# Performance work log

Hardware: AMD Instinct MI355X
Metric: run time of the kernel (lower is better)

Reference implementation:

```python
import jax, jax.numpy as jnp
import numpy as np

N = 50000
E = 800000
IN_C, HID_C, OUT_C = 128, 96, 96
EPS = 1e-5


def setup_inputs() -> dict:
    key = jax.random.key(0)
    ks = jax.random.split(key, 16)
    s = lambda k, shape, fan: jax.random.normal(k, shape, jnp.float32) / np.sqrt(fan)
    inp = {
        "x": jax.random.normal(ks[0], (N, IN_C), jnp.float32),
        "edge_index": jax.random.randint(ks[1], (2, E), 0, N, jnp.int64),
        # GCNConv weights (x @ W then aggregate, bias added after)
        "W1": s(ks[2], (IN_C, HID_C), IN_C), "b1": jnp.zeros((HID_C,), jnp.float32),
        "W2": s(ks[3], (HID_C, HID_C), HID_C), "b2": jnp.zeros((HID_C,), jnp.float32),
        "W3": s(ks[4], (HID_C, OUT_C), HID_C), "b3": jnp.zeros((OUT_C,), jnp.float32),
        # BatchNorm affine params
        "g1": jnp.ones((HID_C,), jnp.float32), "bt1": jnp.zeros((HID_C,), jnp.float32),
        "g2": jnp.ones((HID_C,), jnp.float32), "bt2": jnp.zeros((HID_C,), jnp.float32),
        "g3": jnp.ones((OUT_C,), jnp.float32), "bt3": jnp.zeros((OUT_C,), jnp.float32),
        # MLP head
        "fw1": s(ks[5], (OUT_C, 128), OUT_C), "fb1": jnp.zeros((128,), jnp.float32),
        "fw2": s(ks[6], (128, 64), 128), "fb2": jnp.zeros((64,), jnp.float32),
        "fw3": s(ks[7], (64, 32), 64), "fb3": jnp.zeros((32,), jnp.float32),
        "fw4": s(ks[8], (32, 1), 32), "fb4": jnp.zeros((1,), jnp.float32),
    }
    return inp


def gcn_conv(x, W, b, src, dst, n):
    # PyG GCNConv: h = x @ W; add self-loops; sym-normalized scatter-add; + bias
    h = x @ W  # [N, C]
    deg = jax.ops.segment_sum(jnp.ones(src.shape[0], h.dtype), dst, num_segments=n) + 1.0
    dinv = jax.lax.rsqrt(deg)  # deg >= 1 via self-loop
    norm = dinv[src] * dinv[dst]  # [E]
    agg = jax.ops.segment_sum(h[src] * norm[:, None], dst, num_segments=n)
    return agg + h * (dinv * dinv)[:, None] + b  # self-loop term + bias


def batch_norm(x, g, b):
    m = x.mean(axis=0)
    v = x.var(axis=0)  # biased, as torch BN uses in normalization
    return (x - m) * jax.lax.rsqrt(v + EPS) * g + b


def reference(x, edge_index, W1, b1, W2, b2, W3, b3, g1, bt1, g2, bt2, g3, bt3,
              fw1, fb1, fw2, fb2, fw3, fb3, fw4, fb4):
    src, dst = edge_index[0], edge_index[1]
    n = x.shape[0]
    h = jax.nn.relu(batch_norm(gcn_conv(x, W1, b1, src, dst, n), g1, bt1))
    h = jax.nn.relu(batch_norm(gcn_conv(h, W2, b2, src, dst, n), g2, bt2))
    h = jax.nn.relu(batch_norm(gcn_conv(h, W3, b3, src, dst, n), g3, bt3))
    v = h.mean(axis=0)  # graph mean-pool -> [OUT_C]
    v = jax.nn.relu(v @ fw1 + fb1)  # dropout is identity in eval mode
    v = jax.nn.relu(v @ fw2 + fb2)
    v = jax.nn.relu(v @ fw3 + fb3)
    return v @ fw4 + fb4  # [1]
```

## Files before the change

kernel.cpp:

```cpp
#include <hip/hip_runtime.h>
#include <math.h>

#define NCH 96
#define SCAN_TILE 2048

__global__ void zero_kernel(int* __restrict__ cnt, float* __restrict__ small,
                            int n, int nsmall) {
    int i = blockIdx.x * blockDim.x + threadIdx.x;
    if (i < n) cnt[i] = 0;
    if (i < nsmall) small[i] = 0.0f;
}

__global__ void count_kernel(const int* __restrict__ dst, int* __restrict__ cnt, int E) {
    int e = blockIdx.x * blockDim.x + threadIdx.x;
    if (e < E) atomicAdd(&cnt[dst[e]], 1);
}

__global__ __launch_bounds__(256) void scanA_kernel(const int* __restrict__ cnt,
                                                    int* __restrict__ bsum, int n) {
    int b = blockIdx.x, t = threadIdx.x;
    int base = b * SCAN_TILE;
    int s = 0;
    for (int i = t; i < SCAN_TILE; i += 256) {
        int idx = base + i;
        if (idx < n) s += cnt[idx];
    }
#pragma unroll
    for (int off = 32; off; off >>= 1) s += __shfl_down(s, off, 64);
    __shared__ int red[4];
    if ((t & 63) == 0) red[t >> 6] = s;
    __syncthreads();
    if (t == 0) bsum[b] = red[0] + red[1] + red[2] + red[3];
}

__global__ __launch_bounds__(256) void scanB_kernel(int* __restrict__ bsum,
                                                    int* __restrict__ rowptrN, int nb) {
    int t = threadIdx.x;
    __shared__ int ps[256];
    int v = (t < nb) ? bsum[t] : 0;
    ps[t] = v;
    __syncthreads();
    for (int off = 1; off < 256; off <<= 1) {
        int add = (t >= off) ? ps[t - off] : 0;
        __syncthreads();
        ps[t] += add;
        __syncthreads();
    }
    if (t < nb) bsum[t] = ps[t] - v;
    if (t == nb - 1) rowptrN[0] = ps[t];
}

__global__ __launch_bounds__(256) void scanC_kernel(int* __restrict__ cnt,
                                                    const int* __restrict__ bsum,
                                                    int* __restrict__ rowptr,
                                                    float* __restrict__ dinv, int n) {
    int b = blockIdx.x, t = threadIdx.x;
    int base = b * SCAN_TILE + t * 8;
    int c[8];
    int s = 0;
#pragma unroll
    for (int j = 0; j < 8; ++j) {
        int idx = base + j;
        c[j] = (idx < n) ? cnt[idx] : 0;
        s += c[j];
    }
    __shared__ int ps[256];
    ps[t] = s;
    __syncthreads();
    for (int off = 1; off < 256; off <<= 1) {
        int add = (t >= off) ? ps[t - off] : 0;
        __syncthreads();
        ps[t] += add;
        __syncthreads();
    }
    int run = bsum[b] + ps[t] - s;
#pragma unroll
    for (int j = 0; j < 8; ++j) {
        int idx = base + j;
        if (idx < n) {
            rowptr[idx] = run;
            cnt[idx] = run;
            dinv[idx] = rsqrtf((float)(c[j] + 1));
            run += c[j];
        }
    }
}

__global__ void fill_kernel(const int* __restrict__ ei, int* __restrict__ fill,
                            int* __restrict__ adj, int E) {
    int e = blockIdx.x * blockDim.x + threadIdx.x;
    if (e < E) {
        int s = ei[e];
        int pos = atomicAdd(&fill[ei[E + e]], 1);
        adj[pos] = s;
    }
}

template <int K, bool BN>
__global__ __launch_bounds__(256) void gemm_hs(const float* __restrict__ x,
                                               const float* __restrict__ ab,
                                               const float* __restrict__ W,
                                               const float* __restrict__ dinv,
                                               float* __restrict__ hs, int n) {
    __shared__ float Wl[K * NCH];
    __shared__ float Xl[32 * 32];
    __shared__ float ABl[2 * NCH];
    const int tid = threadIdx.y * 32 + threadIdx.x;
    for (int i = tid; i < K * NCH; i += 256) Wl[i] = W[i];
    if (BN && tid < 2 * NCH) ABl[tid] = ab[tid];

    const int r0 = blockIdx.x * 32;
    const int c0 = threadIdx.x;
    const int ry = threadIdx.y;
    float a[4][3] = {};

    for (int kc = 0; kc < K; kc += 32) {
        __syncthreads();
        for (int i = tid; i < 32 * 32; i += 256) {
            int row = i >> 5, kk = i & 31;
            int r = r0 + row;
            float v = (r < n) ? x[(size_t)r * K + kc + kk] : 0.0f;
            if (BN) v = fmaxf(fmaf(v, ABl[kc + kk], ABl[NCH + kc + kk]), 0.0f);
            Xl[i] = v;
        }
        __syncthreads();
#pragma unroll
        for (int kk = 0; kk < 32; ++kk) {
            float w0 = Wl[(kc + kk) * NCH + c0];
            float w1 = Wl[(kc + kk) * NCH + c0 + 32];
            float w2 = Wl[(kc + kk) * NCH + c0 + 64];
#pragma unroll
            for (int j = 0; j < 4; ++j) {
                float xv = Xl[(ry + 8 * j) * 32 + kk];
                a[j][0] = fmaf(xv, w0, a[j][0]);
                a[j][1] = fmaf(xv, w1, a[j][1]);
                a[j][2] = fmaf(xv, w2, a[j][2]);
            }
        }
    }

#pragma unroll
    for (int j = 0; j < 4; ++j) {
        int r = r0 + ry + 8 * j;
        if (r < n) {
            float dv = dinv[r];
#pragma unroll
            for (int i2 = 0; i2 < 3; ++i2)
                hs[(size_t)r * NCH + c0 + 32 * i2] = a[j][i2] * dv;
        }
    }
}

__global__ __launch_bounds__(256) void gather_kernel(const int* __restrict__ rowptr,
                                                     const int* __restrict__ adj,
                                                     const float* __restrict__ dinv,
                                                     const float4* __restrict__ HS,
                                                     float4* __restrict__ AGG, int n) {
    int wid = (blockIdx.x * 256 + threadIdx.x) >> 6;
    int lane = threadIdx.x & 63;
    if (wid >= n || lane >= 24) return;
    int lo = rowptr[wid], hi = rowptr[wid + 1];
    float dv = dinv[wid];
    size_t l = lane;

    float4 a = HS[(size_t)wid * 24 + l];
    float4 b = make_float4(0.f, 0.f, 0.f, 0.f);
    int j = lo;
    for (; j + 1 < hi; j += 2) {
        int s0 = adj[j], s1 = adj[j + 1];
        float4 v0 = HS[(size_t)s0 * 24 + l];
        float4 v1 = HS[(size_t)s1 * 24 + l];
        a.x += v0.x; a.y += v0.y; a.z += v0.z; a.w += v0.w;
        b.x += v1.x; b.y += v1.y; b.z += v1.z; b.w += v1.w;
    }
    if (j < hi) {
        int s0 = adj[j];
        float4 v0 = HS[(size_t)s0 * 24 + l];
        a.x += v0.x; a.y += v0.y; a.z += v0.z; a.w += v0.w;
    }
    a.x = (a.x + b.x) * dv;
    a.y = (a.y + b.y) * dv;
    a.z = (a.z + b.z) * dv;
    a.w = (a.w + b.w) * dv;
    AGG[(size_t)wid * 24 + l] = a;
}

__global__ __launch_bounds__(384) void stats_kernel(const float* __restrict__ t,
                                                    float* __restrict__ sums, int n) {
    int c = threadIdx.x;
    int ry = threadIdx.y;
    float s1 = 0.f, s2 = 0.f;
    for (int r = blockIdx.x * 4 + ry; r < n; r += gridDim.x * 4) {
        float v = t[(size_t)r * NCH + c];
        s1 += v;
        s2 = fmaf(v, v, s2);
    }
    __shared__ float L1[4][NCH], L2[4][NCH];
    L1[ry][c] = s1;
    L2[ry][c] = s2;
    __syncthreads();
    if (ry == 0) {
        s1 = L1[0][c] + L1[1][c] + L1[2][c] + L1[3][c];
        s2 = L2[0][c] + L2[1][c] + L2[2][c] + L2[3][c];
        atomicAdd(&sums[c], s1);
        atomicAdd(&sums[NCH + c], s2);
    }
}

__global__ void bnparam_kernel(const float* __restrict__ sums,
                               const float* __restrict__ g,
                               const float* __restrict__ bt,
                               float* __restrict__ ab, float n) {
    int c = threadIdx.x;
    if (c < NCH) {
        float mean = sums[c] / n;
        float var = sums[NCH + c] / n - mean * mean;
        float a = g[c] * rsqrtf(var + 1e-5f);
        ab[c] = a;
        ab[NCH + c] = bt[c] - mean * a;
    }
}

__global__ __launch_bounds__(384) void apply_pool_kernel(const float* __restrict__ t,
                                                         const float* __restrict__ ab,
                                                         float* __restrict__ pool, int n) {
    int c = threadIdx.x, ry = threadIdx.y;
    float a = ab[c], b = ab[NCH + c];
    float s = 0.f;
    for (int r = blockIdx.x * 4 + ry; r < n; r += gridDim.x * 4) {
        float v = t[(size_t)r * NCH + c];
        s += fmaxf(fmaf(v, a, b), 0.f);
    }
    __shared__ float L[4][NCH];
    L[ry][c] = s;
    __syncthreads();
    if (ry == 0) atomicAdd(&pool[c], L[0][c] + L[1][c] + L[2][c] + L[3][c]);
}

__global__ __launch_bounds__(128) void mlp_kernel(const float* __restrict__ pool,
        const float* __restrict__ fw1, const float* __restrict__ fb1,
        const float* __restrict__ fw2, const float* __restrict__ fb2,
        const float* __restrict__ fw3, const float* __restrict__ fb3,
        const float* __restrict__ fw4, const float* __restrict__ fb4,
        float* __restrict__ out, float invn) {
    __shared__ float v[NCH], l1[128], l2[64], l3[32];
    int t = threadIdx.x;
    if (t < NCH) v[t] = pool[t] * invn;
    __syncthreads();
    {
        float a = fb1[t];
        for (int k = 0; k < NCH; ++k) a = fmaf(v[k], fw1[k * 128 + t], a);
        l1[t] = fmaxf(a, 0.f);
    }
    __syncthreads();
    if (t < 64) {
        float a = fb2[t];
        for (int k = 0; k < 128; ++k) a = fmaf(l1[k], fw2[k * 64 + t], a);
        l2[t] = fmaxf(a, 0.f);
    }
    __syncthreads();
    if (t < 32) {
        float a = fb3[t];
        for (int k = 0; k < 64; ++k) a = fmaf(l2[k], fw3[k * 32 + t], a);
        l3[t] = fmaxf(a, 0.f);
    }
    __syncthreads();
    if (t == 0) {
        float a = fb4[0];
        for (int k = 0; k < 32; ++k) a = fmaf(l3[k], fw4[k], a);
        out[0] = a;
    }
}

extern "C" void kernel_launch(void* const* d_in, const int* in_sizes, int n_in,
                              void* d_out, int out_size, void* d_ws, size_t ws_size,
                              hipStream_t stream) {
    const float* x  = (const float*)d_in[0];
    const int*  ei  = (const int*)d_in[1];
    const float* W1 = (const float*)d_in[2];
    const float* W2 = (const float*)d_in[4];
    const float* W3 = (const float*)d_in[6];
    const float* g1 = (const float*)d_in[8],  *bt1 = (const float*)d_in[9];
    const float* g2 = (const float*)d_in[10], *bt2 = (const float*)d_in[11];
    const float* g3 = (const float*)d_in[12], *bt3 = (const float*)d_in[13];
    const float* fw1 = (const float*)d_in[14], *fb1 = (const float*)d_in[15];
    const float* fw2 = (const float*)d_in[16], *fb2 = (const float*)d_in[17];
    const float* fw3 = (const float*)d_in[18], *fb3 = (const float*)d_in[19];
    const float* fw4 = (const float*)d_in[20], *fb4 = (const float*)d_in[21];
    float* out = (float*)d_out;

    const int N = in_sizes[0] / 128;
    const int E = in_sizes[1] / 2;
    const size_t n96 = (size_t)N * NCH;

    float* ws    = (float*)d_ws;
    float* B0    = ws;
    float* B1    = B0 + n96;
    float* dinv  = B1 + n96;
    float* sums1 = dinv + N;
    float* sums2 = sums1 + 2 * NCH;
    float* sums3 = sums2 + 2 * NCH;
    float* pool  = sums3 + 2 * NCH;
    float* ab1   = pool + NCH;
    float* ab2   = ab1 + 2 * NCH;
    float* ab3   = ab2 + 2 * NCH;
    int*   cnt   = (int*)(ab3 + 2 * NCH);
    int*   rowptr= cnt + N;
    int*   adj   = rowptr + N + 1;
    int*   bsum  = adj + E;
    const int nsmall = 3 * 2 * NCH + NCH;

    dim3 b96(NCH, 4);
    const int gemmGrid = (N + 31) / 32;
    const int gathGrid = (N + 3) / 4;
    const int nb = (N + SCAN_TILE - 1) / SCAN_TILE;

    zero_kernel<<<(N + 255) / 256, 256, 0, stream>>>(cnt, sums1, N, nsmall);
    count_kernel<<<(E + 255) / 256, 256, 0, stream>>>(ei + E, cnt, E);
    scanA_kernel<<<nb, 256, 0, stream>>>(cnt, bsum, N);
    scanB_kernel<<<1, 256, 0, stream>>>(bsum, rowptr + N, nb);
    scanC_kernel<<<nb, 256, 0, stream>>>(cnt, bsum, rowptr, dinv, N);
    fill_kernel<<<(E + 255) / 256, 256, 0, stream>>>(ei, cnt, adj, E);

    gemm_hs<128, false><<<gemmGrid, dim3(32, 8), 0, stream>>>(x, nullptr, W1, dinv, B0, N);
    gather_kernel<<<gathGrid, 256, 0, stream>>>(rowptr, adj, dinv,
                                                (const float4*)B0, (float4*)B1, N);
    stats_kernel<<<512, b96, 0, stream>>>(B1, sums1, N);
    bnparam_kernel<<<1, NCH, 0, stream>>>(sums1, g1, bt1, ab1, (float)N);

    gemm_hs<96, true><<<gemmGrid, dim3(32, 8), 0, stream>>>(B1, ab1, W2, dinv, B0, N);
    gather_kernel<<<gathGrid, 256, 0, stream>>>(rowptr, adj, dinv,
                                                (const float4*)B0, (float4*)B1, N);
    stats_kernel<<<512, b96, 0, stream>>>(B1, sums2, N);
    bnparam_kernel<<<1, NCH, 0, stream>>>(sums2, g2, bt2, ab2, (float)N);

    gemm_hs<96, true><<<gemmGrid, dim3(32, 8), 0, stream>>>(B1, ab2, W3, dinv, B0, N);
    gather_kernel<<<gathGrid, 256, 0, stream>>>(rowptr, adj, dinv,
                                                (const float4*)B0, (float4*)B1, N);
    stats_kernel<<<512, b96, 0, stream>>>(B1, sums3, N);
    bnparam_kernel<<<1, NCH, 0, stream>>>(sums3, g3, bt3, ab3, (float)N);

    apply_pool_kernel<<<512, b96, 0, stream>>>(B1, ab3, pool, N);
    mlp_kernel<<<1, 128, 0, stream>>>(pool, fw1, fb1, fw2, fb2, fw3, fb3,
                                      fw4, fb4, out, 1.0f / (float)N);
}
```

Measured before the change: 558.9 us.

## Use split-bf16 MFMA for GEMMs and store gathered features as bf16

Replaces the scalar FMA GEMM with an MFMA 16x16x32 bf16 kernel. It uses a three-term hi/lo bf16 split to keep near-fp32 accuracy, with weights pre-swizzled into LDS fragment order and 128 rows per block. The GEMM output h*dinv is now stored as bf16, which halves the bytes the random-access neighbor gather reads. The gather accumulates in fp32 after unpacking. The risk is the precision loss from rounding the gathered features to bf16, plus extra conversion work in the GEMM.

After: 500.1 us. 10.5% less time.

```diff
diff --git a/kernel.cpp b/kernel.cpp
--- a/kernel.cpp
+++ b/kernel.cpp
@@ -3,6 +3,25 @@
 
 #define NCH 96
 #define SCAN_TILE 2048
+
+typedef __attribute__((ext_vector_type(8))) short short8;
+typedef __attribute__((ext_vector_type(4))) float f32x4;
+typedef unsigned short ushort_t;
+typedef unsigned int uint_t;
+
+__device__ __forceinline__ uint_t bf16_rne(float f) {
+    uint_t u = __builtin_bit_cast(uint_t, f);
+    return (u + 0x7FFFu + ((u >> 16) & 1u)) >> 16;
+}
+
+__device__ __forceinline__ float4 unp(uint2 u) {
+    float4 r;
+    r.x = __builtin_bit_cast(float, u.x << 16);
+    r.y = __builtin_bit_cast(float, u.x & 0xFFFF0000u);
+    r.z = __builtin_bit_cast(float, u.y << 16);
+    r.w = __builtin_bit_cast(float, u.y & 0xFFFF0000u);
+    return r;
+}
 
 __global__ void zero_kernel(int* __restrict__ cnt, float* __restrict__ small,
                             int n, int nsmall) {
@@ -97,56 +116,99 @@
 }
 
 template <int K, bool BN>
-__global__ __launch_bounds__(256) void gemm_hs(const float* __restrict__ x,
-                                               const float* __restrict__ ab,
-                                               const float* __restrict__ W,
-                                               const float* __restrict__ dinv,
-                                               float* __restrict__ hs, int n) {
-    __shared__ float Wl[K * NCH];
-    __shared__ float Xl[32 * 32];
+__global__ __launch_bounds__(256) void gemm_mfma(const float* __restrict__ x,
+                                                 const float* __restrict__ ab,
+                                                 const float* __restrict__ W,
+                                                 const float* __restrict__ dinv,
+                                                 ushort_t* __restrict__ hs, int n) {
+    constexpr int NKS = K / 32;
+    constexpr int NFR = NKS * 6 * 512;
+    __shared__ short BH[NFR];
+    __shared__ short BL[NFR];
     __shared__ float ABl[2 * NCH];
-    const int tid = threadIdx.y * 32 + threadIdx.x;
-    for (int i = tid; i < K * NCH; i += 256) Wl[i] = W[i];
-    if (BN && tid < 2 * NCH) ABl[tid] = ab[tid];
-
-    const int r0 = blockIdx.x * 32;
-    const int c0 = threadIdx.x;
-    const int ry = threadIdx.y;
-    float a[4][3] = {};
-
-    for (int kc = 0; kc < K; kc += 32) {
-        __syncthreads();
-        for (int i = tid; i < 32 * 32; i += 256) {
-            int row = i >> 5, kk = i & 31;
-            int r = r0 + row;
-            float v = (r < n) ? x[(size_t)r * K + kc + kk] : 0.0f;
-            if (BN) v = fmaxf(fmaf(v, ABl[kc + kk], ABl[NCH + kc + kk]), 0.0f);
-            Xl[i] = v;
+
+    const int tid = threadIdx.x;
+    for (int idx = tid; idx < NFR; idx += 256) {
+        int i  = idx & 7;
+        int l2 = (idx >> 3) & 63;
+        int r  = idx >> 9;
+        int ct = r % 6;
+        int ks = r / 6;
+        int k   = ks * 32 + ((l2 >> 4) << 3) + i;
+        int col = ct * 16 + (l2 & 15);
+        float w = W[k * NCH + col];
+        uint_t hb = bf16_rne(w);
+        float hf = __builtin_bit_cast(float, hb << 16);
+        uint_t lb = bf16_rne(w - hf);
+        BH[idx] = (short)hb;
+        BL[idx] = (short)lb;
+    }
+    if constexpr (BN) {
+        if (tid < 2 * NCH) ABl[tid] = ab[tid];
+    }
+    __syncthreads();
+
+    const int l  = tid & 63;
+    const int wv = tid >> 6;
+    const int r0 = blockIdx.x * 128 + wv * 32;
+    const int klo = (l >> 4) << 3;
+
+    f32x4 acc[2][6] = {};
+
+    for (int ks = 0; ks < NKS; ++ks) {
+        float av[8], bv[8];
+        if constexpr (BN) {
+            int kb = ks * 32 + klo;
+#pragma unroll
+            for (int i = 0; i < 8; ++i) { av[i] = ABl[kb + i]; bv[i] = ABl[NCH + kb + i]; }
         }
-        __syncthreads();
-#pragma unroll
-        for (int kk = 0; kk < 32; ++kk) {
-            float w0 = Wl[(kc + kk) * NCH + c0];
-            float w1 = Wl[(kc + kk) * NCH + c0 + 32];
-            float w2 = Wl[(kc + kk) * NCH + c0 + 64];
-#pragma unroll
-            for (int j = 0; j < 4; ++j) {
-                float xv = Xl[(ry + 8 * j) * 32 + kk];
-                a[j][0] = fmaf(xv, w0, a[j][0]);
-                a[j][1] = fmaf(xv, w1, a[j][1]);
-                a[j][2] = fmaf(xv, w2, a[j][2]);
+        short8 Ah[2], Al[2];
+#pragma unroll
+        for (int rt = 0; rt < 2; ++rt) {
+            int rg = r0 + rt * 16 + (l & 15);
+            rg = rg < n ? rg : n - 1;
+            const float* px = x + (size_t)rg * K + ks * 32 + klo;
+            float4 f0 = *(const float4*)px;
+            float4 f1 = *(const float4*)(px + 4);
+            float vv[8] = {f0.x, f0.y, f0.z, f0.w, f1.x, f1.y, f1.z, f1.w};
+#pragma unroll
+            for (int i = 0; i < 8; ++i) {
+                float v = vv[i];
+                if constexpr (BN) v = fmaxf(fmaf(v, av[i], bv[i]), 0.0f);
+                uint_t hb = bf16_rne(v);
+                float hf = __builtin_bit_cast(float, hb << 16);
+                uint_t lb = bf16_rne(v - hf);
+                Ah[rt][i] = (short)hb;
+                Al[rt][i] = (short)lb;
             }
         }
-    }
-
-#pragma unroll
-    for (int j = 0; j < 4; ++j) {
-        int r = r0 + ry + 8 * j;
-        if (r < n) {
-            float dv = dinv[r];
-#pragma unroll
-            for (int i2 = 0; i2 < 3; ++i2)
-                hs[(size_t)r * NCH + c0 + 32 * i2] = a[j][i2] * dv;
+#pragma unroll
+        for (int ct = 0; ct < 6; ++ct) {
+            int off = ((ks * 6 + ct) << 9) + (l << 3);
+            short8 bh = *(const short8*)&BH[off];
+            short8 bl = *(const short8*)&BL[off];
+#pragma unroll
+            for (int rt = 0; rt < 2; ++rt) {
+                acc[rt][ct] = __builtin_amdgcn_mfma_f32_16x16x32_bf16(Ah[rt], bh, acc[rt][ct], 0, 0, 0);
+                acc[rt][ct] = __builtin_amdgcn_mfma_f32_16x16x32_bf16(Al[rt], bh, acc[rt][ct], 0, 0, 0);
+                acc[rt][ct] = __builtin_amdgcn_mfma_f32_16x16x32_bf16(Ah[rt], bl, acc[rt][ct], 0, 0, 0);
+            }
+        }
+    }
+
+#pragma unroll
+    for (int rt = 0; rt < 2; ++rt) {
+#pragma unroll
+        for (int i = 0; i < 4; ++i) {
+            int row = r0 + rt * 16 + ((l >> 4) << 2) + i;
+            if (row < n) {
+                float dv = dinv[row];
+#pragma unroll
+                for (int ct = 0; ct < 6; ++ct) {
+                    float v = acc[rt][ct][i] * dv;
+                    hs[(size_t)row * NCH + ct * 16 + (l & 15)] = (ushort_t)bf16_rne(v);
+                }
+            }
         }
     }
 }
@@ -154,35 +216,36 @@
 __global__ __launch_bounds__(256) void gather_kernel(const int* __restrict__ rowptr,
                                                      const int* __restrict__ adj,
                                                      const float* __restrict__ dinv,
-                                                     const float4* __restrict__ HS,
-                                                     float4* __restrict__ AGG, int n) {
+                                                     const ushort_t* __restrict__ HS,
+                                                     float* __restrict__ AGG, int n) {
     int wid = (blockIdx.x * 256 + threadIdx.x) >> 6;
     int lane = threadIdx.x & 63;
     if (wid >= n || lane >= 24) return;
     int lo = rowptr[wid], hi = rowptr[wid + 1];
     float dv = dinv[wid];
-    size_t l = lane;
-
-    float4 a = HS[(size_t)wid * 24 + l];
+    const uint_t* HSu = (const uint_t*)HS;
+    const int l2 = lane * 2;
+
+    float4 a = unp(*(const uint2*)(HSu + (size_t)wid * 48 + l2));
     float4 b = make_float4(0.f, 0.f, 0.f, 0.f);
     int j = lo;
     for (; j + 1 < hi; j += 2) {
         int s0 = adj[j], s1 = adj[j + 1];
-        float4 v0 = HS[(size_t)s0 * 24 + l];
-        float4 v1 = HS[(size_t)s1 * 24 + l];
+        float4 v0 = unp(*(const uint2*)(HSu + (size_t)s0 * 48 + l2));
+        float4 v1 = unp(*(const uint2*)(HSu + (size_t)s1 * 48 + l2));
         a.x += v0.x; a.y += v0.y; a.z += v0.z; a.w += v0.w;
         b.x += v1.x; b.y += v1.y; b.z += v1.z; b.w += v1.w;
     }
     if (j < hi) {
         int s0 = adj[j];
-        float4 v0 = HS[(size_t)s0 * 24 + l];
+        float4 v0 = unp(*(const uint2*)(HSu + (size_t)s0 * 48 + l2));
         a.x += v0.x; a.y += v0.y; a.z += v0.z; a.w += v0.w;
     }
     a.x = (a.x + b.x) * dv;
     a.y = (a.y + b.y) * dv;
     a.z = (a.z + b.z) * dv;
     a.w = (a.w + b.w) * dv;
-    AGG[(size_t)wid * 24 + l] = a;
+    ((float4*)(AGG + (size_t)wid * NCH))[lane] = a;
 }
 
 __global__ __launch_bounds__(384) void stats_kernel(const float* __restrict__ t,
@@ -294,9 +357,9 @@
     const size_t n96 = (size_t)N * NCH;
 
     float* ws    = (float*)d_ws;
-    float* B0    = ws;
-    float* B1    = B0 + n96;
-    float* dinv  = B1 + n96;
+    float* T     = ws;
+    ushort_t* HSB = (ushort_t*)(T + n96);
+    float* dinv  = T + n96 + n96 / 2;
     float* sums1 = dinv + N;
     float* sums2 = sums1 + 2 * NCH;
     float* sums3 = sums2 + 2 * NCH;
@@ -311,7 +374,7 @@
     const int nsmall = 3 * 2 * NCH + NCH;
 
     dim3 b96(NCH, 4);
-    const int gemmGrid = (N + 31) / 32;
+    const int gemmGrid = (N + 127) / 128;
     const int gathGrid = (N + 3) / 4;
     const int nb = (N + SCAN_TILE - 1) / SCAN_TILE;
 
@@ -322,25 +385,22 @@
     scanC_kernel<<<nb, 256, 0, stream>>>(cnt, bsum, rowptr, dinv, N);
     fill_kernel<<<(E + 255) / 256, 256, 0, stream>>>(ei, cnt, adj, E);
 
-    gemm_hs<128, false><<<gemmGrid, dim3(32, 8), 0, stream>>>(x, nullptr, W1, dinv, B0, N);
-    gather_kernel<<<gathGrid, 256, 0, stream>>>(rowptr, adj, dinv,
-                                                (const float4*)B0, (float4*)B1, N);
-    stats_kernel<<<512, b96, 0, stream>>>(B1, sums1, N);
+    gemm_mfma<128, false><<<gemmGrid, 256, 0, stream>>>(x, nullptr, W1, dinv, HSB, N);
+    gather_kernel<<<gathGrid, 256, 0, stream>>>(rowptr, adj, dinv, HSB, T, N);
+    stats_kernel<<<512, b96, 0, stream>>>(T, sums1, N);
     bnparam_kernel<<<1, NCH, 0, stream>>>(sums1, g1, bt1, ab1, (float)N);
 
-    gemm_hs<96, true><<<gemmGrid, dim3(32, 8), 0, stream>>>(B1, ab1, W2, dinv, B0, N);
-    gather_kernel<<<gathGrid, 256, 0, stream>>>(rowptr, adj, dinv,
-                                                (const float4*)B0, (float4*)B1, N);
-    stats_kernel<<<512, b96, 0, stream>>>(B1, sums2, N);
+    gemm_mfma<96, true><<<gemmGrid, 256, 0, stream>>>(T, ab1, W2, dinv, HSB, N);
+    gather_kernel<<<gathGrid, 256, 0, stream>>>(rowptr, adj, dinv, HSB, T, N);
+    stats_kernel<<<512, b96, 0, stream>>>(T, sums2, N);
     bnparam_kernel<<<1, NCH, 0, stream>>>(sums2, g2, bt2, ab2, (float)N);
 
-    gemm_hs<96, true><<<gemmGrid, dim3(32, 8), 0, stream>>>(B1, ab2, W3, dinv, B0, N);
-    gather_kernel<<<gathGrid, 256, 0, stream>>>(rowptr, adj, dinv,
-                                                (const float4*)B0, (float4*)B1, N);
-    stats_kernel<<<512, b96, 0, stream>>>(B1, sums3, N);
+    gemm_mfma<96, true><<<gemmGrid, 256, 0, stream>>>(T, ab2, W3, dinv, HSB, N);
+    gather_kernel<<<gathGrid, 256, 0, stream>>>(rowptr, adj, dinv, HSB, T, N);
+    stats_kernel<<<512, b96, 0, stream>>>(T, sums3, N);
     bnparam_kernel<<<1, NCH, 0, stream>>>(sums3, g3, bt3, ab3, (float)N);
 
-    apply_pool_kernel<<<512, b96, 0, stream>>>(B1, ab3, pool, N);
+    apply_pool_kernel<<<512, b96, 0, stream>>>(T, ab3, pool, N);
     mlp_kernel<<<1, 128, 0, stream>>>(pool, fw1, fb1, fw2, fb2, fw3, fb3,
                                       fw4, fb4, out, 1.0f / (float)N);
 }
```
